# Kernel tuning notes

Measured on AMD Instinct MI355X. Metric: run time of the kernel, lower is better.

## Reference

```python
import jax, jax.numpy as jnp
import numpy as np

N_SUBJECTS = 64
N_LABELS = 16
DENS_TEMP = 0.1  # args.ProtoSim_dens_temp


def setup_inputs() -> dict:
    key = jax.random.key(0)
    k1, k2, k3 = jax.random.split(key, 3)
    B, V, D = 16384, 2, 512
    X_data = jax.random.normal(k1, (B, V, D), dtype=jnp.float32)
    subject = jax.random.randint(k2, (B,), 0, N_SUBJECTS)
    labels = jax.random.randint(k3, (B,), 0, N_LABELS)
    return {"X_data": X_data, "subject": subject, "labels": labels}


def reference(X_data, subject, labels):
    B, V, D = X_data.shape  # V == contrast_count == 2 (code doubles subject/labels once)
    K = N_SUBJECTS * N_LABELS
    # torch.cat(torch.unbind(X, dim=1), dim=0) -> [V*B, D]
    cf = jnp.transpose(X_data, (1, 0, 2)).reshape(V * B, D)
    subj2 = jnp.concatenate([subject, subject])
    lab2 = jnp.concatenate([labels, labels])
    # group id: groups enumerated sorted-by-(subject,label), i.e. g = s*C + l
    gid = subj2 * N_LABELS + lab2
    ones = jnp.ones((V * B,), dtype=cf.dtype)
    counts = jax.ops.segment_sum(ones, gid, num_segments=K)  # [K]
    safe_cnt = jnp.maximum(counts, 1.0)
    centroid = jax.ops.segment_sum(cf, gid, num_segments=K) / safe_cnt[:, None]  # [K, D]
    # per-sample euclidean distance to own group centroid (torch.cdist)
    dist = jnp.linalg.norm(cf - centroid[gid], axis=1)  # [V*B]
    # density_g = mean(sqrt(dist)) / log(n_g + 10) for n_g > 1, else dmax; then clip & scale
    mean_sqrt = jax.ops.segment_sum(jnp.sqrt(dist), gid, num_segments=K) / safe_cnt
    density = mean_sqrt / jnp.log(counts + 10.0)
    density = jnp.where(counts > 1, density, 0.0)
    density = jnp.where(counts > 1, density, density.max())
    density = jnp.clip(density, jnp.percentile(density, 10), jnp.percentile(density, 90))
    density = DENS_TEMP * density / density.mean()
    density = jax.lax.stop_gradient(density)  # torch builds it via .tolist()/numpy
    # mask: different subject AND same label vs each group prototype
    g_subj = jnp.arange(K) // N_LABELS
    g_lab = jnp.arange(K) % N_LABELS
    mask = ((subj2[:, None] != g_subj[None, :]) & (lab2[:, None] == g_lab[None, :])).astype(cf.dtype)  # [V*B, K]
    # with N_SUBJECTS > 1 every row has >= 1 positive group -> no rows deleted
    sim = jnp.matmul(cf, centroid.T) / density[None, :]  # [V*B, K]
    sim = sim - jax.lax.stop_gradient(jnp.max(sim, axis=1, keepdims=True))
    positive_sim = sim * mask
    # CrossEntropyLoss(reduction='none') with soft (unnormalized) targets = mask
    logp = jax.nn.log_softmax(positive_sim, axis=1)
    loss_per_row = -(mask * logp).sum(axis=1) / mask.sum(axis=1)
    return loss_per_row.mean()
```

## Files before the change

### kernel.cpp

```cpp
#include <hip/hip_runtime.h>


typedef __bf16 v8bf __attribute__((ext_vector_type(8)));
typedef __bf16 v4bf __attribute__((ext_vector_type(4)));
typedef float  v4f  __attribute__((ext_vector_type(4)));
typedef unsigned int u32x4 __attribute__((ext_vector_type(4)));

#define B_ROWS 16384
#define ROWS   32768
#define NGRP   1024
#define DIM    512
#define LOG2E  1.4426950408889634f
#define LN2    0.6931471805599453f

__device__ __forceinline__ float wredSum(float v){
#pragma unroll
  for (int o = 32; o > 0; o >>= 1) v += __shfl_xor(v, o);
  return v;
}
__device__ __forceinline__ float wredMax(float v){
#pragma unroll
  for (int o = 32; o > 0; o >>= 1) v = fmaxf(v, __shfl_xor(v, o));
  return v;
}

__global__ void kA2(const int* __restrict__ subj, const int* __restrict__ lab,
                    int* __restrict__ base_cnt, int* __restrict__ gid_arr){
  int i = blockIdx.x * 256 + threadIdx.x;
  int g = subj[i] * 16 + lab[i];
  gid_arr[i] = g;
  atomicAdd(&base_cnt[g], 1);
}

__global__ void kA3(const int* __restrict__ base_cnt, int* __restrict__ offs,
                    int* __restrict__ fillp){
  __shared__ int sb[NGRP];
  int t = threadIdx.x;
  int c = base_cnt[t];
  sb[t] = c;
  __syncthreads();
  for (int off = 1; off < NGRP; off <<= 1){
    int v = (t >= off) ? sb[t - off] : 0;
    __syncthreads();
    sb[t] += v;
    __syncthreads();
  }
  int ex = sb[t] - c;
  offs[t] = ex;
  fillp[t] = ex;
}

__global__ void kA4(const int* __restrict__ gid_arr, int* __restrict__ fillp,
                    int* __restrict__ row_list){
  int i = blockIdx.x * 256 + threadIdx.x;
  int pos = atomicAdd(&fillp[gid_arr[i]], 1);
  row_list[pos] = i;
}

__global__ void kB(const float* __restrict__ X, const int* __restrict__ base_cnt,
                   const int* __restrict__ offs, const int* __restrict__ row_list,
                   float* __restrict__ cent_f, __bf16* __restrict__ cent_b){
  int g = blockIdx.x, t = threadIdx.x;
  int n = base_cnt[g], off = offs[g];
  float ax = 0.f, ay = 0.f, az = 0.f, aw = 0.f;
  for (int j = 0; j < n; ++j){
    int r = row_list[off + j];
    const float4* p = (const float4*)(X + (size_t)r * 1024);
    float4 a = p[t];
    float4 b = p[t + 128];
    ax += a.x + b.x; ay += a.y + b.y; az += a.z + b.z; aw += a.w + b.w;
  }
  int cnt2 = 2 * n;
  float inv = 1.0f / (float)(cnt2 > 1 ? cnt2 : 1);
  float4 c; c.x = ax * inv; c.y = ay * inv; c.z = az * inv; c.w = aw * inv;
  ((float4*)(cent_f + (size_t)g * DIM))[t] = c;
  v4bf cb; cb[0] = (__bf16)c.x; cb[1] = (__bf16)c.y; cb[2] = (__bf16)c.z; cb[3] = (__bf16)c.w;
  *(v4bf*)(cent_b + (size_t)g * DIM + t * 4) = cb;
}

__global__ void kC(const float* __restrict__ X, const int* __restrict__ subj,
                   const int* __restrict__ lab, const float* __restrict__ cent_f,
                   float* __restrict__ msq, __bf16* __restrict__ cfb){
  int w = threadIdx.x >> 6, lane = threadIdx.x & 63;
  int r = blockIdx.x * 4 + w;
  int i = r & (B_ROWS - 1), v = r >> 14;
  int g = subj[i] * 16 + lab[i];
  const float4* xr = (const float4*)(X + ((size_t)(i * 2 + v)) * DIM);
  const float4* cr = (const float4*)(cent_f + (size_t)g * DIM);
  float4 x0 = xr[lane], x1 = xr[lane + 64];
  float4 c0 = cr[lane], c1 = cr[lane + 64];
  float s = 0.f, d;
  d = x0.x - c0.x; s += d * d;  d = x0.y - c0.y; s += d * d;
  d = x0.z - c0.z; s += d * d;  d = x0.w - c0.w; s += d * d;
  d = x1.x - c1.x; s += d * d;  d = x1.y - c1.y; s += d * d;
  d = x1.z - c1.z; s += d * d;  d = x1.w - c1.w; s += d * d;
  v4bf b0; b0[0]=(__bf16)x0.x; b0[1]=(__bf16)x0.y; b0[2]=(__bf16)x0.z; b0[3]=(__bf16)x0.w;
  v4bf b1; b1[0]=(__bf16)x1.x; b1[1]=(__bf16)x1.y; b1[2]=(__bf16)x1.z; b1[3]=(__bf16)x1.w;
  *(v4bf*)(cfb + (size_t)r * DIM + lane * 4)       = b0;
  *(v4bf*)(cfb + (size_t)r * DIM + 256 + lane * 4) = b1;
  s = wredSum(s);
  if (lane == 0){
    float dist = sqrtf(s);
    atomicAdd(&msq[g], sqrtf(dist));
  }
}

__global__ void kD(const int* __restrict__ base_cnt, const float* __restrict__ msq,
                   float* __restrict__ scale2){
  __shared__ float sd[NGRP];
  __shared__ float ss[NGRP];
  __shared__ float rb[16];
  int t = threadIdx.x;
  int lane = t & 63, wid = t >> 6;
  int cnt2 = 2 * base_cnt[t];
  float safe = (float)(cnt2 > 1 ? cnt2 : 1);
  float v = (msq[t] / safe) / logf((float)cnt2 + 10.0f);
  float d1 = (cnt2 > 1) ? v : 0.0f;
  float wm = wredMax(d1);
  if (lane == 0) rb[wid] = wm;
  __syncthreads();
  float x = (lane < 16) ? rb[lane] : -3.0e38f;
  if (wid == 0){ x = wredMax(x); if (lane == 0) rb[0] = x; }
  __syncthreads();
  float dmax = rb[0];
  float d2 = (cnt2 > 1) ? d1 : dmax;
  sd[t] = d2;
  __syncthreads();
  int rank = 0;
  for (int j = 0; j < NGRP; ++j){
    float dj = sd[j];
    rank += (dj < d2) || (dj == d2 && j < t);
  }
  ss[rank] = d2;
  __syncthreads();
  float p10 = ss[102] + 0.3f * (ss[103] - ss[102]);
  float p90 = ss[920] + 0.7f * (ss[921] - ss[920]);
  float c = fminf(fmaxf(d2, p10), p90);
  __syncthreads();
  float wsm = wredSum(c);
  if (lane == 0) rb[wid] = wsm;
  __syncthreads();
  float y = (lane < 16) ? rb[lane] : 0.0f;
  if (wid == 0){ y = wredSum(y); if (lane == 0) rb[0] = y; }
  __syncthreads();
  float mean = rb[0] * (1.0f / 1024.0f);
  scale2[t] = LOG2E * mean / (0.1f * c);
}

__global__ __launch_bounds__(256, 2)
void kE(const __bf16* __restrict__ cfb, const __bf16* __restrict__ centb,
        const float* __restrict__ scale2, const int* __restrict__ gid_arr,
        float* __restrict__ loss_sum){
  __shared__ u32x4 cent[2][128 * 9];
  __shared__ float sscale[NGRP];
  __shared__ float red[4];
  int tid = threadIdx.x, lane = tid & 63, w = tid >> 6;
  int l15 = lane & 15, lhi = lane >> 4;
  int row = blockIdx.x * 64 + w * 16 + l15;

  const u32x4* gA = (const u32x4*)centb;
  const u32x4* gB = (const u32x4*)cfb;

  ((v4f*)sscale)[tid] = ((const v4f*)scale2)[tid];

  u32x4 breg[16];
  {
    const u32x4* rp = gB + (size_t)row * 64 + lhi;
#pragma unroll
    for (int c = 0; c < 16; ++c) breg[c] = rp[c * 4];
  }

  int g = gid_arr[row & (B_ROWS - 1)];
  int rsub = g >> 4, rlab = g & 15;
  float labeq[4];
#pragma unroll
  for (int j = 0; j < 4; ++j) labeq[j] = (rlab == lhi * 4 + j) ? 1.0f : 0.0f;

  u32x4 st[4];
  auto stage = [&](int tt){
    int gb = tt >> 3, ks = tt & 7;
#pragma unroll
    for (int c2 = 0; c2 < 4; ++c2){
      int flat = c2 * 256 + tid;
      int mrow = flat >> 3, kidx = flat & 7;
      st[c2] = gA[(size_t)(gb * 128 + mrow) * 64 + ks * 8 + kidx];
    }
  };
  auto commit = [&](int buf){
#pragma unroll
    for (int c2 = 0; c2 < 4; ++c2){
      int flat = c2 * 256 + tid;
      int mrow = flat >> 3, kidx = flat & 7;
      cent[buf][mrow * 9 + kidx] = st[c2];
    }
  };

  v4f acc[8];
#pragma unroll
  for (int fm = 0; fm < 8; ++fm) acc[fm] = (v4f){0.f, 0.f, 0.f, 0.f};
  float M = -3.0e38f, E = 0.f, S = 0.f;

  stage(0); commit(0);
  __syncthreads();

  for (int gb = 0; gb < 8; ++gb){
#pragma unroll
    for (int ks = 0; ks < 8; ++ks){
      int tt = gb * 8 + ks;
      if (tt < 63) stage(tt + 1);
#pragma unroll
      for (int kk = 0; kk < 2; ++kk){
        v8bf afr[8];
#pragma unroll
        for (int fm = 0; fm < 8; ++fm){
          int mrow = fm * 16 + l15;
          afr[fm] = __builtin_bit_cast(v8bf, cent[ks & 1][mrow * 9 + kk * 4 + lhi]);
        }
#pragma unroll
        for (int fm = 0; fm < 8; ++fm)
          acc[fm] = __builtin_amdgcn_mfma_f32_16x16x32_bf16(
              afr[fm], __builtin_bit_cast(v8bf, breg[ks * 2 + kk]), acc[fm], 0, 0, 0);
      }
      if (tt < 63){
        commit((tt + 1) & 1);
        __syncthreads();
      }
    }
    {
      v4f vs[8];
      float mloc = -3.0e38f;
#pragma unroll
      for (int fm = 0; fm < 8; ++fm){
        v4f sc = *(const v4f*)&sscale[gb * 128 + fm * 16 + lhi * 4];
        v4f t;
#pragma unroll
        for (int j = 0; j < 4; ++j){
          t[j] = acc[fm][j] * sc[j];
          mloc = fmaxf(mloc, t[j]);
        }
        vs[fm] = t;
      }
      float Mn = fmaxf(M, mloc);
      float eadd = 0.f, sadd = 0.f;
#pragma unroll
      for (int fm = 0; fm < 8; ++fm){
        float subne = (rsub != gb * 8 + fm) ? 1.0f : 0.0f;
#pragma unroll
        for (int j = 0; j < 4; ++j){
          float mk = subne * labeq[j];
          eadd += mk * exp2f(vs[fm][j] - Mn);
          sadd += mk * vs[fm][j];
        }
      }
      E = E * exp2f(M - Mn) + eadd;
      S += sadd;
      M = Mn;
#pragma unroll
      for (int fm = 0; fm < 8; ++fm) acc[fm] = (v4f){0.f, 0.f, 0.f, 0.f};
    }
  }

#pragma unroll
  for (int off = 16; off < 64; off <<= 1){
    float mo = __shfl_xor(M, off);
    float eo = __shfl_xor(E, off);
    float so = __shfl_xor(S, off);
    float mn = fmaxf(M, mo);
    E = E * exp2f(M - mn) + eo * exp2f(mo - mn);
    S += so;
    M = mn;
  }
  float loss = logf(961.0f + E) + LN2 * M - LN2 * (S * (1.0f / 63.0f));
  float wsum = wredSum(loss) * 0.25f;
  if (lane == 0) red[w] = wsum;
  __syncthreads();
  if (tid == 0) atomicAdd(loss_sum, red[0] + red[1] + red[2] + red[3]);
}

__global__ void kG(const float* __restrict__ loss_sum, float* __restrict__ out){
  out[0] = loss_sum[0] * (1.0f / (float)ROWS);
}

extern "C" void kernel_launch(void* const* d_in, const int* in_sizes, int n_in,
                              void* d_out, int out_size, void* d_ws, size_t ws_size,
                              hipStream_t stream){
  const float* X   = (const float*)d_in[0];
  const int* subj  = (const int*)d_in[1];
  const int* lab   = (const int*)d_in[2];
  float* out = (float*)d_out;
  char* ws = (char*)d_ws;

  int*    base_cnt = (int*)(ws + 0);
  float*  msq      = (float*)(ws + 4096);
  float*  loss_s   = (float*)(ws + 8192);
  int*    offs     = (int*)(ws + 8448);
  int*    fillp    = (int*)(ws + 12544);
  int*    gid_arr  = (int*)(ws + 16640);
  int*    row_list = (int*)(ws + 82176);
  float*  scale2   = (float*)(ws + 147712);
  float*  cent_f   = (float*)(ws + 151808);
  __bf16* cent_b   = (__bf16*)(ws + 2248960);
  __bf16* cfb      = (__bf16*)(ws + 3297536);

  hipMemsetAsync(ws, 0, 8208, stream);

  kA2<<<64, 256, 0, stream>>>(subj, lab, base_cnt, gid_arr);
  kA3<<<1, 1024, 0, stream>>>(base_cnt, offs, fillp);
  kA4<<<64, 256, 0, stream>>>(gid_arr, fillp, row_list);
  kB <<<1024, 128, 0, stream>>>(X, base_cnt, offs, row_list, cent_f, cent_b);
  kC <<<8192, 256, 0, stream>>>(X, subj, lab, cent_f, msq, cfb);
  kD <<<1, 1024, 0, stream>>>(base_cnt, msq, scale2);
  kE <<<512, 256, 0, stream>>>(cfb, cent_b, scale2, gid_arr, loss_s);
  kG <<<1, 1, 0, stream>>>(loss_s, out);
}
```

Before: 166.8 us.

## Restructure similarity GEMM kernel with 32x32 MFMA, async LDS loads, swizzled tiles

The main loss kernel is rebuilt around 32x32x16 bf16 MFMA instead of 16x16x32. Each wave now holds a full 32-row B fragment and processes half the groups, so two waves share the rows. Centroid tiles are streamed into swizzled LDS with global_load_lds, which bypasses registers. Per-row softmax state from the two halves is merged through shared memory, and the final mean is atomically accumulated straight into the output, which removes the kG launch. The aim is higher MFMA efficiency and fewer register and LDS round-trips. In exchange, the kernel uses more registers (launch bounds drop to 1 block per CU) and larger LDS tiles, and occupancy may fall.

```diff
diff --git a/kernel.cpp b/kernel.cpp
--- a/kernel.cpp
+++ b/kernel.cpp
@@ -4,6 +4,7 @@
 typedef __bf16 v8bf __attribute__((ext_vector_type(8)));
 typedef __bf16 v4bf __attribute__((ext_vector_type(4)));
 typedef float  v4f  __attribute__((ext_vector_type(4)));
+typedef float  v16f __attribute__((ext_vector_type(16)));
 typedef unsigned int u32x4 __attribute__((ext_vector_type(4)));
 
 #define B_ROWS 16384
@@ -22,6 +23,12 @@
 #pragma unroll
   for (int o = 32; o > 0; o >>= 1) v = fmaxf(v, __shfl_xor(v, o));
   return v;
+}
+
+__device__ __forceinline__ void gload16(const void* g, void* lds){
+  __builtin_amdgcn_global_load_lds(
+      (const __attribute__((address_space(1))) void*)g,
+      (__attribute__((address_space(3))) void*)lds, 16, 0, 0);
 }
 
 __global__ void kA2(const int* __restrict__ subj, const int* __restrict__ lab,
@@ -147,138 +154,131 @@
   scale2[t] = LOG2E * mean / (0.1f * c);
 }
 
-__global__ __launch_bounds__(256, 2)
+__global__ __launch_bounds__(256, 1)
 void kE(const __bf16* __restrict__ cfb, const __bf16* __restrict__ centb,
         const float* __restrict__ scale2, const int* __restrict__ gid_arr,
-        float* __restrict__ loss_sum){
-  __shared__ u32x4 cent[2][128 * 9];
+        float* __restrict__ out){
+  __shared__ u32x4 tile[2][2048];
   __shared__ float sscale[NGRP];
-  __shared__ float red[4];
-  int tid = threadIdx.x, lane = tid & 63, w = tid >> 6;
-  int l15 = lane & 15, lhi = lane >> 4;
-  int row = blockIdx.x * 64 + w * 16 + l15;
-
-  const u32x4* gA = (const u32x4*)centb;
-  const u32x4* gB = (const u32x4*)cfb;
+  __shared__ float redM[128], redE[128], redS[128];
+  int tid = threadIdx.x, lane = tid & 63;
+  int w = tid >> 6, rw = w & 1, h = w >> 1;
+  int l31 = lane & 31, lhi = lane >> 5;
+  int row = blockIdx.x * 64 + rw * 32 + l31;
 
   ((v4f*)sscale)[tid] = ((const v4f*)scale2)[tid];
 
-  u32x4 breg[16];
+  u32x4 breg[32];
   {
-    const u32x4* rp = gB + (size_t)row * 64 + lhi;
-#pragma unroll
-    for (int c = 0; c < 16; ++c) breg[c] = rp[c * 4];
-  }
-
-  int g = gid_arr[row & (B_ROWS - 1)];
-  int rsub = g >> 4, rlab = g & 15;
-  float labeq[4];
-#pragma unroll
-  for (int j = 0; j < 4; ++j) labeq[j] = (rlab == lhi * 4 + j) ? 1.0f : 0.0f;
-
-  u32x4 st[4];
-  auto stage = [&](int tt){
-    int gb = tt >> 3, ks = tt & 7;
-#pragma unroll
-    for (int c2 = 0; c2 < 4; ++c2){
-      int flat = c2 * 256 + tid;
-      int mrow = flat >> 3, kidx = flat & 7;
-      st[c2] = gA[(size_t)(gb * 128 + mrow) * 64 + ks * 8 + kidx];
+    const u32x4* rp = (const u32x4*)cfb + (size_t)row * 64 + lhi;
+#pragma unroll
+    for (int m = 0; m < 32; ++m) breg[m] = rp[2 * m];
+  }
+  int g0 = gid_arr[row & (B_ROWS - 1)];
+  int rsub = g0 >> 4, rlab = g0 & 15;
+
+  const char* gsrc = (const char*)centb;
+  auto stage = [&](int t2, int buf){
+    int i2 = t2 >> 3, ks2 = t2 & 7;
+#pragma unroll
+    for (int it = 0; it < 8; ++it){
+      int p = it * 256 + tid;
+      int trow = p >> 3, clin = p & 7;
+      int c = clin ^ (trow & 7);
+      int grow = i2 * 128 + (trow & 127) + ((trow >> 7) << 9);
+      const void* src = gsrc + ((size_t)(grow * 64 + ks2 * 8 + c) << 4);
+      void* dst = (void*)&tile[buf][it * 256 + (w << 6)];
+      gload16(src, dst);
     }
   };
-  auto commit = [&](int buf){
-#pragma unroll
-    for (int c2 = 0; c2 < 4; ++c2){
-      int flat = c2 * 256 + tid;
-      int mrow = flat >> 3, kidx = flat & 7;
-      cent[buf][mrow * 9 + kidx] = st[c2];
+
+  float M = -3.0e38f, E = 0.f, S = 0.f;
+  stage(0, 0);
+  __syncthreads();
+
+  for (int i = 0; i < 4; ++i){
+    v16f acc[4];
+#pragma unroll
+    for (int fm = 0; fm < 4; ++fm)
+#pragma unroll
+      for (int e = 0; e < 16; ++e) acc[fm][e] = 0.f;
+
+    for (int ks = 0; ks < 8; ++ks){
+      int t2 = i * 8 + ks;
+      int buf = t2 & 1;
+      if (t2 < 31) stage(t2 + 1, buf ^ 1);
+#pragma unroll
+      for (int kk = 0; kk < 4; ++kk){
+#pragma unroll
+        for (int fm = 0; fm < 4; ++fm){
+          int tr = h * 128 + fm * 32 + l31;
+          u32x4 af = tile[buf][tr * 8 + ((kk * 2 + lhi) ^ (tr & 7))];
+          acc[fm] = __builtin_amdgcn_mfma_f32_32x32x16_bf16(
+              __builtin_bit_cast(v8bf, af),
+              __builtin_bit_cast(v8bf, breg[ks * 4 + kk]),
+              acc[fm], 0, 0, 0);
+        }
+      }
+      __syncthreads();
     }
-  };
-
-  v4f acc[8];
-#pragma unroll
-  for (int fm = 0; fm < 8; ++fm) acc[fm] = (v4f){0.f, 0.f, 0.f, 0.f};
-  float M = -3.0e38f, E = 0.f, S = 0.f;
-
-  stage(0); commit(0);
-  __syncthreads();
-
-  for (int gb = 0; gb < 8; ++gb){
-#pragma unroll
-    for (int ks = 0; ks < 8; ++ks){
-      int tt = gb * 8 + ks;
-      if (tt < 63) stage(tt + 1);
-#pragma unroll
-      for (int kk = 0; kk < 2; ++kk){
-        v8bf afr[8];
-#pragma unroll
-        for (int fm = 0; fm < 8; ++fm){
-          int mrow = fm * 16 + l15;
-          afr[fm] = __builtin_bit_cast(v8bf, cent[ks & 1][mrow * 9 + kk * 4 + lhi]);
-        }
-#pragma unroll
-        for (int fm = 0; fm < 8; ++fm)
-          acc[fm] = __builtin_amdgcn_mfma_f32_16x16x32_bf16(
-              afr[fm], __builtin_bit_cast(v8bf, breg[ks * 2 + kk]), acc[fm], 0, 0, 0);
-      }
-      if (tt < 63){
-        commit((tt + 1) & 1);
-        __syncthreads();
+
+    float mloc = -3.0e38f;
+#pragma unroll
+    for (int fm = 0; fm < 4; ++fm){
+      int sbase = h * 512 + i * 128 + fm * 32 + lhi * 4;
+#pragma unroll
+      for (int q = 0; q < 4; ++q){
+        v4f sc = *(const v4f*)&sscale[sbase + q * 8];
+#pragma unroll
+        for (int j = 0; j < 4; ++j)
+          mloc = fmaxf(mloc, acc[fm][q * 4 + j] * sc[j]);
       }
     }
-    {
-      v4f vs[8];
-      float mloc = -3.0e38f;
-#pragma unroll
-      for (int fm = 0; fm < 8; ++fm){
-        v4f sc = *(const v4f*)&sscale[gb * 128 + fm * 16 + lhi * 4];
-        v4f t;
+    float Mn = fmaxf(M, mloc);
+    float eadd = 0.f, sadd = 0.f;
+#pragma unroll
+    for (int fm = 0; fm < 4; ++fm){
+      int sbase = h * 512 + i * 128 + fm * 32 + lhi * 4;
+      int gs_base = h * 32 + i * 8 + fm * 2;
+#pragma unroll
+      for (int q = 0; q < 4; ++q){
+        v4f sc = *(const v4f*)&sscale[sbase + q * 8];
+        float subne = ((gs_base + (q >> 1)) != rsub) ? 1.0f : 0.0f;
 #pragma unroll
         for (int j = 0; j < 4; ++j){
-          t[j] = acc[fm][j] * sc[j];
-          mloc = fmaxf(mloc, t[j]);
-        }
-        vs[fm] = t;
-      }
-      float Mn = fmaxf(M, mloc);
-      float eadd = 0.f, sadd = 0.f;
-#pragma unroll
-      for (int fm = 0; fm < 8; ++fm){
-        float subne = (rsub != gb * 8 + fm) ? 1.0f : 0.0f;
-#pragma unroll
-        for (int j = 0; j < 4; ++j){
-          float mk = subne * labeq[j];
-          eadd += mk * exp2f(vs[fm][j] - Mn);
-          sadd += mk * vs[fm][j];
+          int glab = j + ((q & 1) << 3) + (lhi << 2);
+          float mk = (glab == rlab) ? subne : 0.0f;
+          float vv = acc[fm][q * 4 + j] * sc[j];
+          eadd += mk * exp2f(vv - Mn);
+          sadd += mk * vv;
         }
       }
-      E = E * exp2f(M - Mn) + eadd;
-      S += sadd;
-      M = Mn;
-#pragma unroll
-      for (int fm = 0; fm < 8; ++fm) acc[fm] = (v4f){0.f, 0.f, 0.f, 0.f};
     }
-  }
-
-#pragma unroll
-  for (int off = 16; off < 64; off <<= 1){
-    float mo = __shfl_xor(M, off);
-    float eo = __shfl_xor(E, off);
-    float so = __shfl_xor(S, off);
+    E = E * exp2f(M - Mn) + eadd;
+    S += sadd;
+    M = Mn;
+  }
+
+  {
+    float mo = __shfl_xor(M, 32), eo = __shfl_xor(E, 32), so = __shfl_xor(S, 32);
     float mn = fmaxf(M, mo);
     E = E * exp2f(M - mn) + eo * exp2f(mo - mn);
-    S += so;
-    M = mn;
-  }
-  float loss = logf(961.0f + E) + LN2 * M - LN2 * (S * (1.0f / 63.0f));
-  float wsum = wredSum(loss) * 0.25f;
-  if (lane == 0) red[w] = wsum;
-  __syncthreads();
-  if (tid == 0) atomicAdd(loss_sum, red[0] + red[1] + red[2] + red[3]);
-}
-
-__global__ void kG(const float* __restrict__ loss_sum, float* __restrict__ out){
-  out[0] = loss_sum[0] * (1.0f / (float)ROWS);
+    S += so; M = mn;
+  }
+  if (lhi == 0){
+    redM[w * 32 + l31] = M; redE[w * 32 + l31] = E; redS[w * 32 + l31] = S;
+  }
+  __syncthreads();
+  if (tid < 64){
+    float m0 = redM[tid], e0 = redE[tid], s0 = redS[tid];
+    float m1 = redM[tid + 64], e1 = redE[tid + 64], s1 = redS[tid + 64];
+    float mn = fmaxf(m0, m1);
+    float Ee = e0 * exp2f(m0 - mn) + e1 * exp2f(m1 - mn);
+    float Ss = s0 + s1;
+    float loss = logf(961.0f + Ee) + LN2 * mn - LN2 * (Ss * (1.0f / 63.0f));
+    float ws = wredSum(loss);
+    if (tid == 0) atomicAdd(out, ws * (1.0f / (float)ROWS));
+  }
 }
 
 extern "C" void kernel_launch(void* const* d_in, const int* in_sizes, int n_in,
@@ -287,29 +287,27 @@
   const float* X   = (const float*)d_in[0];
   const int* subj  = (const int*)d_in[1];
   const int* lab   = (const int*)d_in[2];
-  float* out = (float*)d_out;
   char* ws = (char*)d_ws;
 
   int*    base_cnt = (int*)(ws + 0);
   float*  msq      = (float*)(ws + 4096);
-  float*  loss_s   = (float*)(ws + 8192);
-  int*    offs     = (int*)(ws + 8448);
-  int*    fillp    = (int*)(ws + 12544);
-  int*    gid_arr  = (int*)(ws + 16640);
-  int*    row_list = (int*)(ws + 82176);
-  float*  scale2   = (float*)(ws + 147712);
-  float*  cent_f   = (float*)(ws + 151808);
-  __bf16* cent_b   = (__bf16*)(ws + 2248960);
-  __bf16* cfb      = (__bf16*)(ws + 3297536);
-
-  hipMemsetAsync(ws, 0, 8208, stream);
+  int*    offs     = (int*)(ws + 8192);
+  int*    fillp    = (int*)(ws + 12288);
+  int*    gid_arr  = (int*)(ws + 16384);
+  int*    row_list = (int*)(ws + 81920);
+  float*  scale2   = (float*)(ws + 147456);
+  float*  cent_f   = (float*)(ws + 151552);
+  __bf16* cent_b   = (__bf16*)(ws + 2248704);
+  __bf16* cfb      = (__bf16*)(ws + 3297280);
+
+  hipMemsetAsync(ws, 0, 8192, stream);
+  hipMemsetAsync(d_out, 0, sizeof(float), stream);
 
   kA2<<<64, 256, 0, stream>>>(subj, lab, base_cnt, gid_arr);
   kA3<<<1, 1024, 0, stream>>>(base_cnt, offs, fillp);
   kA4<<<64, 256, 0, stream>>>(gid_arr, fillp, row_list);
-  kB <<<1024, 128, 0, stream>>>(X, base_cnt, offs, row_list, cent_f, cent_b);
+  kB <<<NGRP, 128, 0, stream>>>(X, base_cnt, offs, row_list, cent_f, cent_b);
   kC <<<8192, 256, 0, stream>>>(X, subj, lab, cent_f, msq, cfb);
   kD <<<1, 1024, 0, stream>>>(base_cnt, msq, scale2);
-  kE <<<512, 256, 0, stream>>>(cfb, cent_b, scale2, gid_arr, loss_s);
-  kG <<<1, 1, 0, stream>>>(loss_s, out);
-}
+  kE <<<512, 256, 0, stream>>>(cfb, cent_b, scale2, gid_arr, (float*)d_out);
+}
```

New measurement: 182.7 us. 1.09x slower.
